# Performance work log

Measured on AMD Instinct MI355X. Metric: run time of the kernel, lower is better.

Reference implementation:

```python
import jax, jax.numpy as jnp
import numpy as np

NUM_HEADS = 16
EPS = 1e-8


def _dyn_quant(x):
    # per-token symmetric int8 quantization (dynamic input scale)
    s = jnp.maximum(jnp.max(jnp.abs(x), axis=-1, keepdims=True) / 127.0, EPS)
    q = jnp.clip(jnp.round(x / s), -127.0, 127.0)
    return q, s


def _quant_weight(w):
    # per-output-channel symmetric int8 weight quantization; w: [out, in]
    s = jnp.maximum(jnp.max(jnp.abs(w), axis=1, keepdims=True) / 127.0, EPS)
    q = jnp.clip(jnp.round(w / s), -127.0, 127.0)
    return q, s


def _w8a8_linear(x, w, b):
    # W8A8 GEMM with int32-exact accumulation (values fit exactly in fp32),
    # dequantized by per-token input scale * per-channel weight scale.
    qx, sx = _dyn_quant(x)          # [B,N,C], [B,N,1]
    qw, sw = _quant_weight(w)       # [O,C],   [O,1]
    y = jnp.einsum('bnc,oc->bno', qx, qw) * (sx * sw[:, 0])
    return y + b


def setup_inputs() -> dict:
    key = jax.random.key(0)
    ks = jax.random.split(key, 9)
    B, N, L, C = 2, 4096, 512, 2048
    sc = 0.02  # realistic weight init scale
    return {
        'x':    jax.random.normal(ks[0], (B, N, C), jnp.float32),
        'cond': jax.random.normal(ks[1], (B, L, C), jnp.float32),
        'mask': jnp.zeros((B, N, L), jnp.float32),  # additive attention mask
        'wq': jax.random.normal(ks[2], (C, C), jnp.float32) * sc,
        'bq': jnp.zeros((C,), jnp.float32),
        'wk': jax.random.normal(ks[3], (C, C), jnp.float32) * sc,
        'bk': jnp.zeros((C,), jnp.float32),
        'wv': jax.random.normal(ks[4], (C, C), jnp.float32) * sc,
        'bv': jnp.zeros((C,), jnp.float32),
        'wo': jax.random.normal(ks[5], (C, C), jnp.float32) * sc,
        'bo': jnp.zeros((C,), jnp.float32),
    }


def reference(x, cond, mask, wq, bq, wk, bk, wv, bv, wo, bo):
    B, N, C = x.shape
    L = cond.shape[1]
    H = NUM_HEADS
    D = C // H
    inv_sqrt_d = np.float32(1.0 / np.sqrt(D))

    # quantized Q projection, fp K/V projections
    q = _w8a8_linear(x, wq, bq).reshape(B, N, H, D).transpose(0, 2, 1, 3)      # [B,H,N,D]
    k = (cond @ wk.T + bk).reshape(B, L, H, D).transpose(0, 2, 1, 3)           # [B,H,L,D]
    v = (cond @ wv.T + bv).reshape(B, L, H, D).transpose(0, 2, 1, 3)           # [B,H,L,D]

    # SDPA cross-attention with additive mask broadcast over heads
    scores = jnp.einsum('bhnd,bhld->bhnl', q, k) * inv_sqrt_d + mask[:, None]
    attn = jax.nn.softmax(scores, axis=-1)
    o = jnp.einsum('bhnl,bhld->bhnd', attn, v)
    o = o.transpose(0, 2, 1, 3).reshape(B, N, C)

    # fused quant_sum (per-token requant) + quantized output projection
    return _w8a8_linear(o, wo, bo)
```

## Files before the change

### kernel.cpp

```cpp
#include <hip/hip_runtime.h>
#include <cstdint>
#include <cstddef>


typedef __bf16 bf16;
typedef __bf16 bf16x8 __attribute__((ext_vector_type(8)));
typedef __bf16 bf16x4 __attribute__((ext_vector_type(4)));
typedef float  f32x4  __attribute__((ext_vector_type(4)));
typedef int    i32x4  __attribute__((ext_vector_type(4)));

#define DEV __device__ __forceinline__

static constexpr int CB = 2;
static constexpr int CN = 4096;
static constexpr int CL = 512;
static constexpr int CC = 2048;
static constexpr int CH = 16;
static constexpr int CD = 128;
static constexpr int TOK = CB * CN;
static constexpr int LR  = CB * CL;

DEV void gl_lds16(const void* g, void* l) {
  __builtin_amdgcn_global_load_lds(
      (const __attribute__((address_space(1))) unsigned int*)g,
      (__attribute__((address_space(3))) unsigned int*)l, 16, 0, 0);
}

DEV f32x4 mfma16(bf16x8 a, bf16x8 b, f32x4 c) {
  return __builtin_amdgcn_mfma_f32_16x16x32_bf16(a, b, c, 0, 0, 0);
}

DEV i32x4 mfma_i8(i32x4 a, i32x4 b, i32x4 c) {
  return __builtin_amdgcn_mfma_i32_16x16x64_i8(a, b, c, 0, 0, 0);
}

__global__ __launch_bounds__(256) void quant_rows_i8(
    const float* __restrict__ in, signed char* __restrict__ q,
    float* __restrict__ scale)
{
  const int r = blockIdx.x, t = threadIdx.x;
  const float* x = in + (size_t)r * CC;
  const float4 v0 = ((const float4*)x)[2 * t];
  const float4 v1 = ((const float4*)x)[2 * t + 1];
  float m = fmaxf(fmaxf(fmaxf(fabsf(v0.x), fabsf(v0.y)), fmaxf(fabsf(v0.z), fabsf(v0.w))),
                  fmaxf(fmaxf(fabsf(v1.x), fabsf(v1.y)), fmaxf(fabsf(v1.z), fabsf(v1.w))));
#pragma unroll
  for (int off = 32; off > 0; off >>= 1) m = fmaxf(m, __shfl_xor(m, off));
  __shared__ float sm[4];
  if ((t & 63) == 0) sm[t >> 6] = m;
  __syncthreads();
  m = fmaxf(fmaxf(sm[0], sm[1]), fmaxf(sm[2], sm[3]));
  const float s = fmaxf(m / 127.0f, 1e-8f);
  if (t == 0) scale[r] = s;
  const float a[8] = {v0.x, v0.y, v0.z, v0.w, v1.x, v1.y, v1.z, v1.w};
  int2 pk;
  int lo = 0, hi = 0;
#pragma unroll
  for (int j = 0; j < 4; j++) {
    const int b0 = (int)fminf(fmaxf(rintf(a[j]     / s), -127.f), 127.f);
    const int b1 = (int)fminf(fmaxf(rintf(a[4 + j] / s), -127.f), 127.f);
    lo |= (b0 & 255) << (8 * j);
    hi |= (b1 & 255) << (8 * j);
  }
  pk.x = lo; pk.y = hi;
  const int c0 = t * 8;
  const int f = (r >> 1) & 3;
  const int pos = (c0 & ~63) | ((((c0 >> 4) & 3) ^ f) << 4) | (c0 & 15);
  *(int2*)&q[(size_t)r * CC + pos] = pk;
}

__global__ __launch_bounds__(256) void split_pair_k(
    const float* __restrict__ in, bf16* __restrict__ hi, bf16* __restrict__ lo)
{
  const size_t i = (size_t)blockIdx.x * 256 + threadIdx.x;
  const float4 v = ((const float4*)in)[i];
  const float a[4] = {v.x, v.y, v.z, v.w};
  bf16x4 h4, l4;
#pragma unroll
  for (int j = 0; j < 4; j++) {
    bf16 h = (bf16)a[j];
    h4[j] = h;
    l4[j] = (bf16)(a[j] - (float)h);
  }
  ((bf16x4*)hi)[i] = h4;
  ((bf16x4*)lo)[i] = l4;
}

__global__ __launch_bounds__(256) void bias_split_k(
    const float* __restrict__ in, const float* __restrict__ bias,
    bf16* __restrict__ hi, bf16* __restrict__ lo)
{
  const size_t i = (size_t)blockIdx.x * 256 + threadIdx.x;
  const float4 v = ((const float4*)in)[i];
  const float4 bb = ((const float4*)bias)[i & (CC / 4 - 1)];
  const float a[4] = {v.x + bb.x, v.y + bb.y, v.z + bb.z, v.w + bb.w};
  bf16x4 h4, l4;
#pragma unroll
  for (int j = 0; j < 4; j++) {
    bf16 h = (bf16)a[j];
    h4[j] = h;
    l4[j] = (bf16)(a[j] - (float)h);
  }
  ((bf16x4*)hi)[i] = h4;
  ((bf16x4*)lo)[i] = l4;
}

__global__ __launch_bounds__(256) void bias_split_vt_k(
    const float* __restrict__ Vf, const float* __restrict__ bias,
    bf16* __restrict__ vth, bf16* __restrict__ vtl)
{
  __shared__ float tile[32][33];
  const int t = threadIdx.x;
  const int l0 = blockIdx.x * 32, d0 = blockIdx.y * 32, bh = blockIdx.z;
  const int b = bh >> 4, h = bh & 15;
  const int r = t >> 3, c4 = (t & 7) * 4;
  const float4 v = *(const float4*)&Vf[((size_t)b * CL + l0 + r) * CC + h * CD + d0 + c4];
  const float4 bb = *(const float4*)&bias[h * CD + d0 + c4];
  tile[r][c4 + 0] = v.x + bb.x;
  tile[r][c4 + 1] = v.y + bb.y;
  tile[r][c4 + 2] = v.z + bb.z;
  tile[r][c4 + 3] = v.w + bb.w;
  __syncthreads();
  bf16x4 h4, l4;
#pragma unroll
  for (int j = 0; j < 4; j++) {
    const float a = tile[c4 + j][r];
    const bf16 hh = (bf16)a;
    h4[j] = hh;
    l4[j] = (bf16)(a - (float)hh);
  }
  const size_t o = ((size_t)bh * CD + d0 + r) * CL + l0 + c4;
  *(bf16x4*)&vth[o] = h4;
  *(bf16x4*)&vtl[o] = l4;
}

template <int MODE>
__global__ __launch_bounds__(256) void gemm_i8(
    const signed char* __restrict__ A, const signed char* __restrict__ B,
    float* __restrict__ out0, bf16* __restrict__ outH, bf16* __restrict__ outL,
    const float* __restrict__ rowS, const float* __restrict__ colS,
    const float* __restrict__ bias, const int Nd, const int K)
{
  __shared__ signed char sA[2][128 * 64] __attribute__((aligned(16)));
  __shared__ signed char sB[2][128 * 64] __attribute__((aligned(16)));
  const int t = threadIdx.x;
  int lin = blockIdx.y * 16 + blockIdx.x;
  lin = (lin & 7) * 128 + (lin >> 3);
  const int m0 = (lin >> 4) * 128, n0 = (lin & 15) * 128;
  const int srow = t >> 2, scol = (t & 3) * 16;
  const signed char* aP = A + (size_t)(m0 + srow) * K + scol;
  const signed char* bP = B + (size_t)(n0 + srow) * K + scol;
  const int lane = t & 63, wave = t >> 6;
  const int wm = (wave >> 1) * 64, wn = (wave & 1) * 64;
  const int quad = lane >> 4, l16 = lane & 15;
  i32x4 acc[4][4] = {};

  gl_lds16(aP,                  &sA[0][t * 16]);
  gl_lds16(aP + (size_t)64 * K, &sA[0][4096 + t * 16]);
  gl_lds16(bP,                  &sB[0][t * 16]);
  gl_lds16(bP + (size_t)64 * K, &sB[0][4096 + t * 16]);
  __syncthreads();

  int cur = 0;
  for (int kb = 0; kb < K; kb += 64) {
    const int nx = kb + 64;
    if (nx < K) {
      gl_lds16(aP + nx,                  &sA[cur ^ 1][t * 16]);
      gl_lds16(aP + nx + (size_t)64 * K, &sA[cur ^ 1][4096 + t * 16]);
      gl_lds16(bP + nx,                  &sB[cur ^ 1][t * 16]);
      gl_lds16(bP + nx + (size_t)64 * K, &sB[cur ^ 1][4096 + t * 16]);
    }
    i32x4 fa[4], fb[4];
#pragma unroll
    for (int i = 0; i < 4; i++) {
      const int ra = wm + i * 16 + l16;
      const int rb = wn + i * 16 + l16;
      fa[i] = *(const i32x4*)&sA[cur][ra * 64 + (quad ^ ((ra >> 1) & 3)) * 16];
      fb[i] = *(const i32x4*)&sB[cur][rb * 64 + (quad ^ ((rb >> 1) & 3)) * 16];
    }
#pragma unroll
    for (int mt = 0; mt < 4; mt++)
#pragma unroll
      for (int nt = 0; nt < 4; nt++)
        acc[mt][nt] = mfma_i8(fa[mt], fb[nt], acc[mt][nt]);
    __syncthreads();
    cur ^= 1;
  }

#pragma unroll
  for (int mt = 0; mt < 4; mt++)
#pragma unroll
    for (int nt = 0; nt < 4; nt++)
#pragma unroll
      for (int rg = 0; rg < 4; rg++) {
        const int mr = m0 + wm + mt * 16 + quad * 4 + rg;
        const int nc = n0 + wn + nt * 16 + l16;
        const float a = (float)acc[mt][nt][rg];
        const float sc = rowS[mr] * colS[nc];
        const float v = a * sc + bias[nc];
        if (MODE == 0) {
          out0[(size_t)mr * Nd + nc] = v;
        } else {
          const bf16 h = (bf16)v;
          outH[(size_t)mr * Nd + nc] = h;
          outL[(size_t)mr * Nd + nc] = (bf16)(v - (float)h);
        }
      }
}

__global__ __launch_bounds__(256) void gemm_kv(
    const bf16* __restrict__ Ah, const bf16* __restrict__ Al,
    const bf16* __restrict__ B0h, const bf16* __restrict__ B0l,
    const bf16* __restrict__ B1h, const bf16* __restrict__ B1l,
    float* __restrict__ out0, float* __restrict__ out1,
    const int Nd, const int K, const int kLen)
{
  __shared__ bf16 sAh[128 * 32] __attribute__((aligned(16)));
  __shared__ bf16 sBh[128 * 32] __attribute__((aligned(16)));
  __shared__ bf16 sAl[128 * 32] __attribute__((aligned(16)));
  __shared__ bf16 sBl[128 * 32] __attribute__((aligned(16)));
  const int t = threadIdx.x;
  int lin = (blockIdx.z * 8 + blockIdx.y) * 16 + blockIdx.x;
  lin = (lin & 7) * 128 + (lin >> 3);
  const int bx = lin & 15, by = (lin >> 4) & 7, bz = lin >> 7;
  const int kv = bz >> 2, chunk = bz & 3;
  const bf16* Bh = kv ? B1h : B0h;
  const bf16* Bl = kv ? B1l : B0l;
  float* outF = kv ? out1 : out0;
  const int m0 = by * 128, n0 = bx * 128;
  const int k0 = chunk * kLen;
  const int srow = t >> 2, scol = (t & 3) * 8;
  const bf16* aP  = Ah + (size_t)(m0 + srow) * K + k0 + scol;
  const bf16* bP  = Bh + (size_t)(n0 + srow) * K + k0 + scol;
  const bf16* aPl = Al + (size_t)(m0 + srow) * K + k0 + scol;
  const bf16* bPl = Bl + (size_t)(n0 + srow) * K + k0 + scol;
  const int lane = t & 63, wave = t >> 6;
  const int wm = (wave >> 1) * 64, wn = (wave & 1) * 64;
  const int quad = lane >> 4, l16 = lane & 15;
  f32x4 acc[4][4] = {};

  for (int kb = 0; kb < kLen; kb += 32) {
    __syncthreads();
    gl_lds16(aP + kb,                   &sAh[t * 8]);
    gl_lds16(aP + kb + (size_t)64 * K,  &sAh[2048 + t * 8]);
    gl_lds16(bP + kb,                   &sBh[t * 8]);
    gl_lds16(bP + kb + (size_t)64 * K,  &sBh[2048 + t * 8]);
    gl_lds16(aPl + kb,                  &sAl[t * 8]);
    gl_lds16(aPl + kb + (size_t)64 * K, &sAl[2048 + t * 8]);
    gl_lds16(bPl + kb,                  &sBl[t * 8]);
    gl_lds16(bPl + kb + (size_t)64 * K, &sBl[2048 + t * 8]);
    __syncthreads();
    bf16x8 fa[4], fb[4], fal[4], fbl[4];
#pragma unroll
    for (int i = 0; i < 4; i++) {
      fa[i]  = *(const bf16x8*)&sAh[(wm + i * 16 + l16) * 32 + quad * 8];
      fb[i]  = *(const bf16x8*)&sBh[(wn + i * 16 + l16) * 32 + quad * 8];
      fal[i] = *(const bf16x8*)&sAl[(wm + i * 16 + l16) * 32 + quad * 8];
      fbl[i] = *(const bf16x8*)&sBl[(wn + i * 16 + l16) * 32 + quad * 8];
    }
#pragma unroll
    for (int mt = 0; mt < 4; mt++)
#pragma unroll
      for (int nt = 0; nt < 4; nt++) {
        f32x4 c = acc[mt][nt];
        c = mfma16(fa[mt],  fb[nt],  c);
        c = mfma16(fa[mt],  fbl[nt], c);
        c = mfma16(fal[mt], fb[nt],  c);
        acc[mt][nt] = c;
      }
  }

#pragma unroll
  for (int mt = 0; mt < 4; mt++)
#pragma unroll
    for (int nt = 0; nt < 4; nt++)
#pragma unroll
      for (int rg = 0; rg < 4; rg++) {
        const int mr = m0 + wm + mt * 16 + quad * 4 + rg;
        const int nc = n0 + wn + nt * 16 + l16;
        atomicAdd(&outF[(size_t)mr * Nd + nc], acc[mt][nt][rg]);
      }
}

__global__ __launch_bounds__(512, 4) void attn_k(
    const bf16* __restrict__ qh, const bf16* __restrict__ ql,
    const bf16* __restrict__ kh, const bf16* __restrict__ kl,
    const bf16* __restrict__ vth, const bf16* __restrict__ vtl,
    const float* __restrict__ mask, float* __restrict__ O)
{
  __shared__ char arena[17408 + 20480 + 18432] __attribute__((aligned(16)));
  bf16 (*ks)[32][136] = (bf16 (*)[32][136])arena;
  bf16 (*vt)[128][40] = (bf16 (*)[128][40])(arena + 17408);
  float (*ps)[16][36] = (float (*)[16][36])(arena + 17408 + 20480);
  const int t = threadIdx.x, lane = t & 63, w = t >> 6;
  const int quad = lane >> 4, l16 = lane & 15;
  int lin = (blockIdx.z * 16 + blockIdx.y) * 32 + blockIdx.x;
  lin = (lin & 7) * 128 + (lin >> 3);
  const int n0 = (lin & 31) * 128;
  const int h  = (lin >> 5) & 15;
  const int b  = lin >> 9;
  const int bh = b * CH + h;
  const size_t qrow0 = (size_t)b * CN + n0;
  const float* mrow_base = mask + ((size_t)b * CN + n0 + w * 16 + quad * 4) * CL;

  const int krow = t >> 4, ksg = t & 15;
  const int vrow = t >> 2, vsg = t & 3;
  uint4 krh, krl, vrh, vrl;
  {
    const size_t gro = ((size_t)b * CL + krow) * CC + h * CD + ksg * 8;
    krh = *(const uint4*)(kh + gro);
    krl = *(const uint4*)(kl + gro);
    const size_t gvo = ((size_t)bh * CD + vrow) * CL + vsg * 8;
    vrh = *(const uint4*)(vth + gvo);
    vrl = *(const uint4*)(vtl + gvo);
  }

  bf16x8 qfh[4], qfl[4];
  {
    bf16* qs = (bf16*)arena;
    const int row = t >> 2, sg = t & 3;
    {
      const bf16* src = qh + (qrow0 + row) * CC + h * CD + sg * 32;
      bf16* dst = qs + row * 136 + sg * 32;
#pragma unroll
      for (int j = 0; j < 4; j++) ((uint4*)dst)[j] = ((const uint4*)src)[j];
    }
    __syncthreads();
#pragma unroll
    for (int s = 0; s < 4; s++)
      qfh[s] = *(const bf16x8*)&qs[(w * 16 + l16) * 136 + s * 32 + quad * 8];
    __syncthreads();
    {
      const bf16* src = ql + (qrow0 + row) * CC + h * CD + sg * 32;
      bf16* dst = qs + row * 136 + sg * 32;
#pragma unroll
      for (int j = 0; j < 4; j++) ((uint4*)dst)[j] = ((const uint4*)src)[j];
    }
    __syncthreads();
#pragma unroll
    for (int s = 0; s < 4; s++)
      qfl[s] = *(const bf16x8*)&qs[(w * 16 + l16) * 136 + s * 32 + quad * 8];
  }

  f32x4 oacc[8] = {};
  f32x4 suma = {};
  const bf16 one = (bf16)1.0f;
  const bf16x8 ones = {one, one, one, one, one, one, one, one};
  const float isd = 0.08838834764831845f;

  for (int lc = 0; lc < CL; lc += 32) {
    __syncthreads();
    *(uint4*)&ks[0][krow][ksg * 8] = krh;
    *(uint4*)&ks[1][krow][ksg * 8] = krl;
    {
      const int vc = (vsg ^ ((vrow >> 3) & 3)) * 8;
      *(uint4*)&vt[0][vrow][vc] = vrh;
      *(uint4*)&vt[1][vrow][vc] = vrl;
    }
    __syncthreads();

    float mcur[2][4];
#pragma unroll
    for (int rg = 0; rg < 4; rg++) {
      const float* mrp = mrow_base + (size_t)rg * CL + lc;
      mcur[0][rg] = mrp[l16];
      mcur[1][rg] = mrp[16 + l16];
    }
    const int lcn = lc + 32;
    if (lcn < CL) {
      const size_t gro = ((size_t)b * CL + lcn + krow) * CC + h * CD + ksg * 8;
      krh = *(const uint4*)(kh + gro);
      krl = *(const uint4*)(kl + gro);
    }

    f32x4 sacc[2] = {};
    __builtin_amdgcn_s_setprio(1);
#pragma unroll
    for (int s = 0; s < 4; s++) {
#pragma unroll
      for (int lt = 0; lt < 2; lt++) {
        bf16x8 kbh = *(const bf16x8*)&ks[0][lt * 16 + l16][s * 32 + quad * 8];
        bf16x8 kbl = *(const bf16x8*)&ks[1][lt * 16 + l16][s * 32 + quad * 8];
        sacc[lt] = mfma16(qfh[s], kbh, sacc[lt]);
        sacc[lt] = mfma16(qfh[s], kbl, sacc[lt]);
        sacc[lt] = mfma16(qfl[s], kbh, sacc[lt]);
      }
    }
    __builtin_amdgcn_s_setprio(0);

    float u[2][4];
#pragma unroll
    for (int rg = 0; rg < 4; rg++) {
      u[0][rg] = __expf(sacc[0][rg] * isd + mcur[0][rg]);
      u[1][rg] = __expf(sacc[1][rg] * isd + mcur[1][rg]);
    }

    if (lcn < CL) {
      const size_t gvo = ((size_t)bh * CD + vrow) * CL + lcn + vsg * 8;
      vrh = *(const uint4*)(vth + gvo);
      vrl = *(const uint4*)(vtl + gvo);
    }

#pragma unroll
    for (int lt = 0; lt < 2; lt++)
#pragma unroll
      for (int rg = 0; rg < 4; rg++)
        ps[w][quad * 4 + rg][lt * 16 + l16] = u[lt][rg];
    const float4 p0 = *(const float4*)&ps[w][l16][quad * 8];
    const float4 p1 = *(const float4*)&ps[w][l16][quad * 8 + 4];
    const float pv[8] = {p0.x, p0.y, p0.z, p0.w, p1.x, p1.y, p1.z, p1.w};
    bf16x8 ph, pl;
#pragma unroll
    for (int j = 0; j < 8; j++) {
      bf16 hh = (bf16)pv[j];
      ph[j] = hh;
      pl[j] = (bf16)(pv[j] - (float)hh);
    }

    suma = mfma16(ph, ones, suma);
    suma = mfma16(pl, ones, suma);
    __builtin_amdgcn_s_setprio(1);
#pragma unroll
    for (int nt = 0; nt < 8; nt++) {
      const int vr = nt * 16 + l16;
      const int vsw = (quad ^ ((vr >> 3) & 3)) * 8;
      bf16x8 vbh = *(const bf16x8*)&vt[0][vr][vsw];
      bf16x8 vbl = *(const bf16x8*)&vt[1][vr][vsw];
      f32x4 c = oacc[nt];
      c = mfma16(ph, vbh, c);
      c = mfma16(ph, vbl, c);
      c = mfma16(pl, vbh, c);
      oacc[nt] = c;
    }
    __builtin_amdgcn_s_setprio(0);
  }

  f32x4 inv;
#pragma unroll
  for (int rg = 0; rg < 4; rg++) inv[rg] = 1.0f / suma[rg];
#pragma unroll
  for (int nt = 0; nt < 8; nt++)
#pragma unroll
    for (int rg = 0; rg < 4; rg++) {
      const size_t row = qrow0 + w * 16 + quad * 4 + rg;
      O[row * CC + h * CD + nt * 16 + l16] = oacc[nt][rg] * inv[rg];
    }
}

extern "C" void kernel_launch(void* const* d_in, const int* in_sizes, int n_in,
                              void* d_out, int out_size, void* d_ws, size_t ws_size,
                              hipStream_t stream)
{
  (void)in_sizes; (void)n_in; (void)out_size; (void)ws_size;
  const float* x    = (const float*)d_in[0];
  const float* cond = (const float*)d_in[1];
  const float* mask = (const float*)d_in[2];
  const float* wq   = (const float*)d_in[3];
  const float* bq   = (const float*)d_in[4];
  const float* wk   = (const float*)d_in[5];
  const float* bk   = (const float*)d_in[6];
  const float* wv   = (const float*)d_in[7];
  const float* bv   = (const float*)d_in[8];
  const float* wo   = (const float*)d_in[9];
  const float* bo   = (const float*)d_in[10];
  float* out = (float*)d_out;

  char* wsb = (char*)d_ws;
  size_t off = 0;
  auto alloc = [&](size_t bytes) -> char* {
    char* p = wsb + off;
    off += (bytes + 255) & ~(size_t)255;
    return p;
  };
  signed char* qx  = (signed char*)alloc((size_t)TOK * CC);
  signed char* qwq = (signed char*)alloc((size_t)CC * CC);
  bf16* ch  = (bf16*)alloc((size_t)LR * CC * 2);
  bf16* cl_ = (bf16*)alloc((size_t)LR * CC * 2);
  bf16* wkh = (bf16*)alloc((size_t)CC * CC * 2);
  bf16* wkl = (bf16*)alloc((size_t)CC * CC * 2);
  bf16* wvh = (bf16*)alloc((size_t)CC * CC * 2);
  bf16* wvl = (bf16*)alloc((size_t)CC * CC * 2);
  float* Kf = (float*)alloc((size_t)LR * CC * 4);
  float* Vf = (float*)alloc((size_t)LR * CC * 4);
  float* Obuf = (float*)qx;
  bf16* qhb = (bf16*)alloc((size_t)TOK * CC * 2);
  bf16* qlb = (bf16*)alloc((size_t)TOK * CC * 2);
  bf16* khb = (bf16*)alloc((size_t)LR * CC * 2);
  bf16* klb = (bf16*)alloc((size_t)LR * CC * 2);
  bf16* vth = (bf16*)alloc((size_t)LR * CC * 2);
  bf16* vtl = (bf16*)alloc((size_t)LR * CC * 2);
  signed char* qwo = (signed char*)alloc((size_t)CC * CC);
  float* sx  = (float*)alloc((size_t)TOK * 4);
  float* swq = (float*)alloc((size_t)CC * 4);
  float* swo = (float*)alloc((size_t)CC * 4);
  float* sO  = (float*)alloc((size_t)TOK * 4);
  signed char* qO = (signed char*)qhb;

  quant_rows_i8<<<CC,  256, 0, stream>>>(wq, qwq, swq);
  quant_rows_i8<<<CC,  256, 0, stream>>>(wo, qwo, swo);
  quant_rows_i8<<<TOK, 256, 0, stream>>>(x, qx, sx);
  split_pair_k<<<(LR * CC / 4) / 256, 256, 0, stream>>>(cond, ch, cl_);
  split_pair_k<<<(CC * CC / 4) / 256, 256, 0, stream>>>(wk, wkh, wkl);
  split_pair_k<<<(CC * CC / 4) / 256, 256, 0, stream>>>(wv, wvh, wvl);
  gemm_i8<1><<<dim3(CC / 128, TOK / 128, 1), 256, 0, stream>>>(
      qx, qwq, nullptr, qhb, qlb, sx, swq, bq, CC, CC);
  (void)hipMemsetAsync(Kf, 0, (size_t)LR * CC * 4 * 2, stream);
  gemm_kv<<<dim3(CC / 128, LR / 128, 8), 256, 0, stream>>>(
      ch, cl_, wkh, wkl, wvh, wvl, Kf, Vf, CC, CC, 512);
  bias_split_k<<<(LR * CC / 4) / 256, 256, 0, stream>>>(Kf, bk, khb, klb);
  bias_split_vt_k<<<dim3(CL / 32, CD / 32, CB * CH), 256, 0, stream>>>(Vf, bv, vth, vtl);
  attn_k<<<dim3(CN / 128, CH, CB), 512, 0, stream>>>(
      qhb, qlb, khb, klb, vth, vtl, mask, Obuf);
  quant_rows_i8<<<TOK, 256, 0, stream>>>(Obuf, qO, sO);
  gemm_i8<0><<<dim3(CC / 128, TOK / 128, 1), 256, 0, stream>>>(
      qO, qwo, out, nullptr, nullptr, sO, swo, bo, CC, CC);
}
```

Before: 548.2 us.

## Double-buffer K/V tiles in LDS and widen attention blocks to 256 queries

The attention kernel now runs 1024-thread blocks, each covering 256 query rows, so every K/V tile staged in LDS is reused by twice as many rows. K/V chunks are double-buffered in LDS with loads issued two chunks ahead, which removes one barrier per iteration. The hi/lo bf16 planes are split across the two halves of the block, so each thread moves one plane. In exchange, LDS use per block roughly doubles and the larger block may cut occupancy or add register pressure.

New measurement: 553.9 us. About the same (+1.0%).

```diff
diff --git a/kernel.cpp b/kernel.cpp
--- a/kernel.cpp
+++ b/kernel.cpp
@@ -282,38 +282,36 @@
       }
 }
 
-__global__ __launch_bounds__(512, 4) void attn_k(
+__global__ __launch_bounds__(1024, 4) void attn_k(
     const bf16* __restrict__ qh, const bf16* __restrict__ ql,
     const bf16* __restrict__ kh, const bf16* __restrict__ kl,
     const bf16* __restrict__ vth, const bf16* __restrict__ vtl,
     const float* __restrict__ mask, float* __restrict__ O)
 {
-  __shared__ char arena[17408 + 20480 + 18432] __attribute__((aligned(16)));
-  bf16 (*ks)[32][136] = (bf16 (*)[32][136])arena;
-  bf16 (*vt)[128][40] = (bf16 (*)[128][40])(arena + 17408);
-  float (*ps)[16][36] = (float (*)[16][36])(arena + 17408 + 20480);
+  __shared__ char arena[34816 + 32768 + 36864] __attribute__((aligned(16)));
+  bf16 (*ksb)[2][32][136] = (bf16 (*)[2][32][136])arena;
+  bf16 (*vtb)[2][128][32] = (bf16 (*)[2][128][32])(arena + 34816);
+  float (*ps)[16][36] = (float (*)[16][36])(arena + 34816 + 32768);
   const int t = threadIdx.x, lane = t & 63, w = t >> 6;
   const int quad = lane >> 4, l16 = lane & 15;
-  int lin = (blockIdx.z * 16 + blockIdx.y) * 32 + blockIdx.x;
-  lin = (lin & 7) * 128 + (lin >> 3);
-  const int n0 = (lin & 31) * 128;
-  const int h  = (lin >> 5) & 15;
-  const int b  = lin >> 9;
+  int lin = (blockIdx.z * 16 + blockIdx.y) * 16 + blockIdx.x;
+  lin = (lin & 7) * 64 + (lin >> 3);
+  const int n0 = (lin & 15) * 256;
+  const int h  = (lin >> 4) & 15;
+  const int b  = lin >> 8;
   const int bh = b * CH + h;
   const size_t qrow0 = (size_t)b * CN + n0;
   const float* mrow_base = mask + ((size_t)b * CN + n0 + w * 16 + quad * 4) * CL;
 
-  const int krow = t >> 4, ksg = t & 15;
-  const int vrow = t >> 2, vsg = t & 3;
-  uint4 krh, krl, vrh, vrl;
-  {
-    const size_t gro = ((size_t)b * CL + krow) * CC + h * CD + ksg * 8;
-    krh = *(const uint4*)(kh + gro);
-    krl = *(const uint4*)(kl + gro);
-    const size_t gvo = ((size_t)bh * CD + vrow) * CL + vsg * 8;
-    vrh = *(const uint4*)(vth + gvo);
-    vrl = *(const uint4*)(vtl + gvo);
-  }
+  const int pl   = t >> 9;
+  const int krow = (t >> 4) & 31, ksg = t & 15;
+  const int vrow = (t >> 2) & 127, vsg = t & 3;
+  const bf16* kPsrc = pl ? kl : kh;
+  const bf16* vPsrc = pl ? vtl : vth;
+  const int vc = (vsg ^ ((vrow >> 3) & 3)) * 8;
+  uint4 kr, vr;
+  kr = *(const uint4*)(kPsrc + ((size_t)b * CL + krow) * CC + h * CD + ksg * 8);
+  vr = *(const uint4*)(vPsrc + ((size_t)bh * CD + vrow) * CL + vsg * 8);
 
   bf16x8 qfh[4], qfl[4];
   {
@@ -340,7 +338,13 @@
 #pragma unroll
     for (int s = 0; s < 4; s++)
       qfl[s] = *(const bf16x8*)&qs[(w * 16 + l16) * 136 + s * 32 + quad * 8];
-  }
+    __syncthreads();
+  }
+
+  *(uint4*)&ksb[0][pl][krow][ksg * 8] = kr;
+  *(uint4*)&vtb[0][pl][vrow][vc] = vr;
+  kr = *(const uint4*)(kPsrc + ((size_t)b * CL + 32 + krow) * CC + h * CD + ksg * 8);
+  vr = *(const uint4*)(vPsrc + ((size_t)bh * CD + vrow) * CL + 32 + vsg * 8);
 
   f32x4 oacc[8] = {};
   f32x4 suma = {};
@@ -348,17 +352,19 @@
   const bf16x8 ones = {one, one, one, one, one, one, one, one};
   const float isd = 0.08838834764831845f;
 
-  for (int lc = 0; lc < CL; lc += 32) {
-    __syncthreads();
-    *(uint4*)&ks[0][krow][ksg * 8] = krh;
-    *(uint4*)&ks[1][krow][ksg * 8] = krl;
-    {
-      const int vc = (vsg ^ ((vrow >> 3) & 3)) * 8;
-      *(uint4*)&vt[0][vrow][vc] = vrh;
-      *(uint4*)&vt[1][vrow][vc] = vrl;
-    }
-    __syncthreads();
-
+  for (int ci = 0; ci < CL / 32; ci++) {
+    const int cur = ci & 1;
+    __syncthreads();
+    if (ci + 1 < CL / 32) {
+      *(uint4*)&ksb[cur ^ 1][pl][krow][ksg * 8] = kr;
+      *(uint4*)&vtb[cur ^ 1][pl][vrow][vc] = vr;
+    }
+    if (ci + 2 < CL / 32) {
+      const int lcn = (ci + 2) * 32;
+      kr = *(const uint4*)(kPsrc + ((size_t)b * CL + lcn + krow) * CC + h * CD + ksg * 8);
+      vr = *(const uint4*)(vPsrc + ((size_t)bh * CD + vrow) * CL + lcn + vsg * 8);
+    }
+    const int lc = ci * 32;
     float mcur[2][4];
 #pragma unroll
     for (int rg = 0; rg < 4; rg++) {
@@ -366,12 +372,6 @@
       mcur[0][rg] = mrp[l16];
       mcur[1][rg] = mrp[16 + l16];
     }
-    const int lcn = lc + 32;
-    if (lcn < CL) {
-      const size_t gro = ((size_t)b * CL + lcn + krow) * CC + h * CD + ksg * 8;
-      krh = *(const uint4*)(kh + gro);
-      krl = *(const uint4*)(kl + gro);
-    }
 
     f32x4 sacc[2] = {};
     __builtin_amdgcn_s_setprio(1);
@@ -379,8 +379,8 @@
     for (int s = 0; s < 4; s++) {
 #pragma unroll
       for (int lt = 0; lt < 2; lt++) {
-        bf16x8 kbh = *(const bf16x8*)&ks[0][lt * 16 + l16][s * 32 + quad * 8];
-        bf16x8 kbl = *(const bf16x8*)&ks[1][lt * 16 + l16][s * 32 + quad * 8];
+        bf16x8 kbh = *(const bf16x8*)&ksb[cur][0][lt * 16 + l16][s * 32 + quad * 8];
+        bf16x8 kbl = *(const bf16x8*)&ksb[cur][1][lt * 16 + l16][s * 32 + quad * 8];
         sacc[lt] = mfma16(qfh[s], kbh, sacc[lt]);
         sacc[lt] = mfma16(qfh[s], kbl, sacc[lt]);
         sacc[lt] = mfma16(qfl[s], kbh, sacc[lt]);
@@ -393,12 +393,6 @@
     for (int rg = 0; rg < 4; rg++) {
       u[0][rg] = __expf(sacc[0][rg] * isd + mcur[0][rg]);
       u[1][rg] = __expf(sacc[1][rg] * isd + mcur[1][rg]);
-    }
-
-    if (lcn < CL) {
-      const size_t gvo = ((size_t)bh * CD + vrow) * CL + lcn + vsg * 8;
-      vrh = *(const uint4*)(vth + gvo);
-      vrl = *(const uint4*)(vtl + gvo);
     }
 
 #pragma unroll
@@ -409,27 +403,27 @@
     const float4 p0 = *(const float4*)&ps[w][l16][quad * 8];
     const float4 p1 = *(const float4*)&ps[w][l16][quad * 8 + 4];
     const float pv[8] = {p0.x, p0.y, p0.z, p0.w, p1.x, p1.y, p1.z, p1.w};
-    bf16x8 ph, pl;
+    bf16x8 ph, plv;
 #pragma unroll
     for (int j = 0; j < 8; j++) {
       bf16 hh = (bf16)pv[j];
       ph[j] = hh;
-      pl[j] = (bf16)(pv[j] - (float)hh);
+      plv[j] = (bf16)(pv[j] - (float)hh);
     }
 
     suma = mfma16(ph, ones, suma);
-    suma = mfma16(pl, ones, suma);
+    suma = mfma16(plv, ones, suma);
     __builtin_amdgcn_s_setprio(1);
 #pragma unroll
     for (int nt = 0; nt < 8; nt++) {
-      const int vr = nt * 16 + l16;
-      const int vsw = (quad ^ ((vr >> 3) & 3)) * 8;
-      bf16x8 vbh = *(const bf16x8*)&vt[0][vr][vsw];
-      bf16x8 vbl = *(const bf16x8*)&vt[1][vr][vsw];
+      const int vrr = nt * 16 + l16;
+      const int vsw = (quad ^ ((vrr >> 3) & 3)) * 8;
+      bf16x8 vbh = *(const bf16x8*)&vtb[cur][0][vrr][vsw];
+      bf16x8 vbl = *(const bf16x8*)&vtb[cur][1][vrr][vsw];
       f32x4 c = oacc[nt];
       c = mfma16(ph, vbh, c);
       c = mfma16(ph, vbl, c);
-      c = mfma16(pl, vbh, c);
+      c = mfma16(plv, vbh, c);
       oacc[nt] = c;
     }
     __builtin_amdgcn_s_setprio(0);
@@ -509,7 +503,7 @@
       ch, cl_, wkh, wkl, wvh, wvl, Kf, Vf, CC, CC, 512);
   bias_split_k<<<(LR * CC / 4) / 256, 256, 0, stream>>>(Kf, bk, khb, klb);
   bias_split_vt_k<<<dim3(CL / 32, CD / 32, CB * CH), 256, 0, stream>>>(Vf, bv, vth, vtl);
-  attn_k<<<dim3(CN / 128, CH, CB), 512, 0, stream>>>(
+  attn_k<<<dim3(CN / 256, CH, CB), 1024, 0, stream>>>(
       qhb, qlb, khb, klb, vth, vtl, mask, Obuf);
   quant_rows_i8<<<TOK, 256, 0, stream>>>(Obuf, qO, sO);
   gemm_i8<0><<<dim3(CC / 128, TOK / 128, 1), 256, 0, stream>>>(
```
